# Kernel optimization log

Hardware: AMD Instinct MI355X
Metric: run time of the kernel (lower is better)

## Reference

```python
import jax, jax.numpy as jnp
import numpy as np

IMG_B, IMG_H, IMG_W, IMG_C = 16, 512, 1024, 3

def _base_grid(B, H, W):
    # replicates the module's custom normalization: arange/dim * 2 - 1
    base_x = (jnp.arange(W, dtype=jnp.float32) / W) * 2.0 - 1.0   # [W]
    base_y = (jnp.arange(H, dtype=jnp.float32) / H) * 2.0 - 1.0   # [H]
    base = jnp.stack([jnp.broadcast_to(base_x[None, :], (H, W)),
                      jnp.broadcast_to(base_y[:, None], (H, W))], axis=-1)  # [H,W,2]
    return jnp.broadcast_to(base[None], (B, H, W, 2))

def _grid_sample_bilinear_zeros(im, grid):
    # im: [B,C,H,W], grid: [B,Ho,Wo,2] in [-1,1], align_corners=False, zeros padding
    B, C, H, W = im.shape
    gx, gy = grid[..., 0], grid[..., 1]
    ix = ((gx + 1.0) * W - 1.0) * 0.5
    iy = ((gy + 1.0) * H - 1.0) * 0.5
    x0 = jnp.floor(ix); y0 = jnp.floor(iy)
    wx1 = ix - x0; wx0 = 1.0 - wx1
    wy1 = iy - y0; wy0 = 1.0 - wy1
    x0i = x0.astype(jnp.int32); y0i = y0.astype(jnp.int32)
    b_idx = jnp.arange(B, dtype=jnp.int32)[:, None, None]

    def corner(xi, yi, w):
        valid = (xi >= 0) & (xi < W) & (yi >= 0) & (yi < H)
        xc = jnp.clip(xi, 0, W - 1); yc = jnp.clip(yi, 0, H - 1)
        # advanced indexing -> [B,Ho,Wo,C]
        v = im[b_idx, :, yc, xc]
        return v * (w * valid.astype(im.dtype))[..., None]

    out = (corner(x0i,     y0i,     wx0 * wy0) +
           corner(x0i + 1, y0i,     wx1 * wy0) +
           corner(x0i,     y0i + 1, wx0 * wy1) +
           corner(x0i + 1, y0i + 1, wx1 * wy1))           # [B,Ho,Wo,C]
    return jnp.transpose(out, (0, 3, 1, 2))                # [B,C,Ho,Wo]

def setup_inputs() -> dict:
    key = jax.random.key(0)
    k1, k2, k3 = jax.random.split(key, 3)
    pred_flow = jax.random.normal(k1, (IMG_B, IMG_H, IMG_W, 2), dtype=jnp.float32) * 8.0
    im1_origin = jax.random.uniform(k2, (IMG_B, IMG_C, IMG_H, IMG_W), dtype=jnp.float32)
    im2_origin = jax.random.uniform(k3, (IMG_B, IMG_C, IMG_H, IMG_W), dtype=jnp.float32)
    return {"pred_flow": pred_flow, "im1_origin": im1_origin, "im2_origin": im2_origin}

def reference(pred_flow, im1_origin, im2_origin):
    B, H, W, _ = pred_flow.shape
    scale = jnp.array([W, H], dtype=pred_flow.dtype)
    grid = pred_flow / scale + _base_grid(B, H, W)
    im1_warp = _grid_sample_bilinear_zeros(im1_origin, grid)
    loss = jnp.sum(jnp.abs(im2_origin - im1_warp)) / (W * H)
    return loss
```

## Files before the change

kernel.cpp:

```cpp
#include <hip/hip_runtime.h>
#include <hip/hip_fp16.h>

namespace {

constexpr int B = 16, C = 3, H = 512, W = 1024;
constexpr int HW = H * W;
constexpr int SLABW = 256, SLABH = 64;
constexpr int XH  = 16;
constexpr int SWD = SLABW + 2 * XH;
constexpr int PAIRS = SWD / 2;
constexpr int PADP = 147;
constexpr int RING = 32;
constexpr int RA = 11;
constexpr int RB = 16;
constexpr int RPS = 4;
constexpr int BLOCK = 1024;
constexpr int TX = W / SLABW;
constexpr int TY = H / SLABH;
constexpr int GRID = B * TX * TY;
constexpr int PF_ROWS = RA + RB + 1;
constexpr int STG_P = C * RPS * PAIRS;
constexpr int CHS = RING * PADP;

constexpr float INV_W = 1.0f / 1024.0f;
constexpr float INV_H = 1.0f / 512.0f;

__device__ __forceinline__ float2 ld2g(const float* p) {
    struct __attribute__((packed, aligned(4))) F2 { float a, b; };
    const F2 v = *reinterpret_cast<const F2*>(p);
    return make_float2(v.a, v.b);
}

__device__ __forceinline__ uint32_t packh2(float a, float b) {
    return (uint32_t)__half_as_ushort(__float2half_rn(a))
         | ((uint32_t)__half_as_ushort(__float2half_rn(b)) << 16);
}
__device__ __forceinline__ float2 unpackh2(uint32_t u) {
    const __half2 h = __builtin_bit_cast(__half2, u);
    return make_float2(__low2float(h), __high2float(h));
}
__device__ __forceinline__ uint32_t alignsel(uint32_t hi, uint32_t lo, int sh) {
    return (uint32_t)(((((uint64_t)hi) << 32) | (uint64_t)lo) >> sh);
}

__global__ __launch_bounds__(BLOCK, 8) void flow_loss_partial(
    const float* __restrict__ flow,
    const float* __restrict__ im1,
    const float* __restrict__ im2,
    float* __restrict__ partials)
{
    __shared__ uint32_t sm32[C * CHS];
    __shared__ float red[BLOCK / 64];

    const int tid = threadIdx.x;
    const int bid = blockIdx.x;
    const int b   = bid >> 5;
    const int tt  = bid & 31;
    const int tyi = tt >> 2;
    const int txi = tt & 3;
    const int xbase  = txi * SLABW;
    const int yStart = tyi * SLABH;
    const int xb0    = xbase - XH;

    const float* __restrict__ im1b = im1 + b * C * HW;
    const float* __restrict__ im2b = im2 + b * C * HW;
    const float* __restrict__ flb  = flow + 2 * (b * HW);

    for (int e = tid; e < PF_ROWS * C * PAIRS; e += BLOCK) {
        const int q  = e % PAIRS;
        const int rc = e / PAIRS;
        const int c  = rc / PF_ROWS;
        const int ri = rc - c * PF_ROWS;
        const int row = yStart - RA + ri;
        if (row >= 0) {
            const int g0 = min(max(xb0 + 2 * q, 0), W - 1);
            const int g1 = min(max(xb0 + 2 * q + 1, 0), W - 1);
            const float a = im1b[c * HW + row * W + g0];
            const float d = im1b[c * HW + row * W + g1];
            sm32[c * CHS + (row & (RING - 1)) * PADP + q] = packh2(a, d);
        }
    }

    int  stSr[2], stG0[2], stG1[2], stL[2];
    const bool stOK1 = (tid < STG_P - BLOCK);
#pragma unroll
    for (int k = 0; k < 2; ++k) {
        const int e  = (k == 0) ? tid : (stOK1 ? BLOCK + tid : 0);
        const int q  = e % PAIRS;
        const int rc = e / PAIRS;
        const int c  = rc >> 2;
        stSr[k] = rc & 3;
        const int g0 = min(max(xb0 + 2 * q, 0), W - 1);
        const int g1 = min(max(xb0 + 2 * q + 1, 0), W - 1);
        stG0[k] = c * HW + g0;
        stG1[k] = c * HW + g1;
        stL[k]  = c * CHS + q;
    }

    auto issue = [&](int r0, int (&sIdx)[2], uint32_t (&sVal)[2]) {
#pragma unroll
        for (int k = 0; k < 2; ++k) {
            const int srow = r0 + stSr[k];
            int idx = -1; uint32_t v = 0;
            const bool act = (k == 0 || stOK1) & (srow < H);
            if (act) {
                const float a = im1b[stG0[k] + (srow << 10)];
                const float d = im1b[stG1[k] + (srow << 10)];
                v   = packh2(a, d);
                idx = stL[k] + (srow & (RING - 1)) * PADP;
            }
            sIdx[k] = idx; sVal[k] = v;
        }
    };

    int sIA[2]; uint32_t sVA[2];
    issue(yStart + RB + 1, sIA, sVA);

    const int colp = tid & (SLABW - 1);
    const int prow = tid >> 8;
    const int x = xbase + colp;
    const float base_x = (float)x * (2.0f * INV_W) - 1.0f;

    __syncthreads();

    float acc = 0.0f;

#pragma unroll 1
    for (int ys = yStart; ys < yStart + SLABH; ys += RPS) {
        int sIB[2]; uint32_t sVB[2];
        issue(ys + RB + 1 + RPS, sIB, sVB);

        const int y = ys + prow;
        const int zoff = y * W + x;
        const float2 f = *reinterpret_cast<const float2*>(flb + 2 * zoff);

        const float base_y = (float)y * (2.0f * INV_H) - 1.0f;
        const float gx = __builtin_fmaf(f.x, INV_W, base_x);
        const float gy = __builtin_fmaf(f.y, INV_H, base_y);
        const float ixf = __builtin_fmaf(gx + 1.0f, 512.0f, -0.5f);
        const float iyf = __builtin_fmaf(gy + 1.0f, 256.0f, -0.5f);

        const float x0f = floorf(ixf), y0f = floorf(iyf);
        const float wx1 = ixf - x0f, wx0 = 1.0f - wx1;
        const float wy1 = iyf - y0f, wy0 = 1.0f - wy1;
        const int x0 = (int)x0f, y0 = (int)y0f;
        const int y1 = y0 + 1;
        const bool vx0 = (x0 >= 0) & (x0 < W);
        const bool vx1 = (x0 >= -1) & (x0 < W - 1);
        const bool vy0 = (y0 >= 0) & (y0 < H);
        const bool vy1 = (y1 >= 0) & (y1 < H);
        const bool s0 = (x0 >= W - 1), s1 = (x0 >= 0);

        const float px0 = wx0 * (float)vx0;
        const float px1 = wx1 * (float)vx1;
        const float u0 = (s0 ? 0.0f : px0) + (s1 ? 0.0f : px1);
        const float u1 = (s0 ? px0 : 0.0f) + (s1 ? px1 : 0.0f);
        const float mT = wy0 * (float)vy0;
        const float mB = wy1 * (float)vy1;
        const float aT0 = mT * u0, aT1 = mT * u1;
        const float aB0 = mB * u0, aB1 = mB * u1;

        const int xL  = min(max(x0, 0), W - 2);
        const int y0c = min(max(y0, 0), H - 1);
        const int y1c = min(max(y1, 0), H - 1);

        const int jj = xL - xbase + XH;
        const bool inR = (y0c >= ys - RA) & (y1c <= ys + RB) &
                         ((unsigned)jj <= (unsigned)(SWD - 2));

        const float z0 = im2b[zoff];
        const float z1 = im2b[HW + zoff];
        const float z2 = im2b[2 * HW + zoff];

        float wp0, wp1, wp2;
        if (inR) {
            const int q  = jj >> 1;
            const int sh = (jj & 1) << 4;
            const int aT = (y0c & (RING - 1)) * PADP + q;
            const int aB = (y1c & (RING - 1)) * PADP + q;
            const uint32_t dT0a = sm32[aT],           dT0b = sm32[aT + 1];
            const uint32_t dB0a = sm32[aB],           dB0b = sm32[aB + 1];
            const uint32_t dT1a = sm32[aT + CHS],     dT1b = sm32[aT + CHS + 1];
            const uint32_t dB1a = sm32[aB + CHS],     dB1b = sm32[aB + CHS + 1];
            const uint32_t dT2a = sm32[aT + 2 * CHS], dT2b = sm32[aT + 2 * CHS + 1];
            const uint32_t dB2a = sm32[aB + 2 * CHS], dB2b = sm32[aB + 2 * CHS + 1];
            const float2 t0 = unpackh2(alignsel(dT0b, dT0a, sh));
            const float2 b0 = unpackh2(alignsel(dB0b, dB0a, sh));
            const float2 t1 = unpackh2(alignsel(dT1b, dT1a, sh));
            const float2 b1 = unpackh2(alignsel(dB1b, dB1a, sh));
            const float2 t2 = unpackh2(alignsel(dT2b, dT2a, sh));
            const float2 b2 = unpackh2(alignsel(dB2b, dB2a, sh));
            wp0 = ((aT0 * t0.x + aT1 * t0.y) + aB0 * b0.x) + aB1 * b0.y;
            wp1 = ((aT0 * t1.x + aT1 * t1.y) + aB0 * b1.x) + aB1 * b1.y;
            wp2 = ((aT0 * t2.x + aT1 * t2.y) + aB0 * b2.x) + aB1 * b2.y;
        } else {
            const int oT = y0c * W + xL, oB = y1c * W + xL;
            const float2 ta = ld2g(im1b + oT),            ba = ld2g(im1b + oB);
            const float2 tb = ld2g(im1b + HW + oT),       bb = ld2g(im1b + HW + oB);
            const float2 tc = ld2g(im1b + 2 * HW + oT),   bc = ld2g(im1b + 2 * HW + oB);
            wp0 = ((aT0 * ta.x + aT1 * ta.y) + aB0 * ba.x) + aB1 * ba.y;
            wp1 = ((aT0 * tb.x + aT1 * tb.y) + aB0 * bb.x) + aB1 * bb.y;
            wp2 = ((aT0 * tc.x + aT1 * tc.y) + aB0 * bc.x) + aB1 * bc.y;
        }
        acc += fabsf(z0 - wp0) + fabsf(z1 - wp1) + fabsf(z2 - wp2);

#pragma unroll
        for (int k = 0; k < 2; ++k)
            if (sIA[k] >= 0) sm32[sIA[k]] = sVA[k];
        __syncthreads();

#pragma unroll
        for (int k = 0; k < 2; ++k) { sIA[k] = sIB[k]; sVA[k] = sVB[k]; }
    }

#pragma unroll
    for (int o = 32; o > 0; o >>= 1)
        acc += __shfl_down(acc, o, 64);
    const int lane = tid & 63;
    const int wid  = tid >> 6;
    if (lane == 0) red[wid] = acc;
    __syncthreads();
    if (tid == 0) {
        float s = 0.0f;
#pragma unroll
        for (int wv = 0; wv < BLOCK / 64; ++wv) s += red[wv];
        partials[bid] = s;
    }
}

__global__ __launch_bounds__(256) void flow_loss_reduce(
    const float* __restrict__ partials, float* __restrict__ out)
{
    __shared__ double lds[256];
    double acc = 0.0;
    for (int i = threadIdx.x; i < GRID; i += 256) acc += (double)partials[i];
    lds[threadIdx.x] = acc;
    __syncthreads();
    for (int o = 128; o > 0; o >>= 1) {
        if (threadIdx.x < o) lds[threadIdx.x] += lds[threadIdx.x + o];
        __syncthreads();
    }
    if (threadIdx.x == 0) out[0] = (float)(lds[0] / (double)(W * H));
}

}

extern "C" void kernel_launch(void* const* d_in, const int* in_sizes, int n_in,
                              void* d_out, int out_size, void* d_ws, size_t ws_size,
                              hipStream_t stream) {
    const float* flow = (const float*)d_in[0];
    const float* im1  = (const float*)d_in[1];
    const float* im2  = (const float*)d_in[2];
    float* out = (float*)d_out;
    float* partials = (float*)d_ws;

    flow_loss_partial<<<GRID, BLOCK, 0, stream>>>(flow, im1, im2, partials);
    flow_loss_reduce<<<1, 256, 0, stream>>>(partials, out);
}
```

Before: 58.80 us.

## Interleave channels in LDS ring buffer for 128-bit loads and stores

Moves the shared-memory ring from three separate per-channel planes to an interleaved layout: each column pair holds all three channels' packed half2 values in one 16-byte slot. The bilinear gather now does four 128-bit LDS reads instead of twelve 32-bit reads, and staging and prefetch write one uint4 per pair while fetching all channels per thread. Padding the 4th word raises LDS footprint by a third and may change bank-conflict behaviour and occupancy.

```diff
diff --git a/kernel.cpp b/kernel.cpp
--- a/kernel.cpp
+++ b/kernel.cpp
@@ -9,7 +9,8 @@
 constexpr int XH  = 16;
 constexpr int SWD = SLABW + 2 * XH;
 constexpr int PAIRS = SWD / 2;
-constexpr int PADP = 147;
+constexpr int QSTR  = 4;
+constexpr int ROWSTR = PAIRS * QSTR + 4;
 constexpr int RING = 32;
 constexpr int RA = 11;
 constexpr int RB = 16;
@@ -19,8 +20,7 @@
 constexpr int TY = H / SLABH;
 constexpr int GRID = B * TX * TY;
 constexpr int PF_ROWS = RA + RB + 1;
-constexpr int STG_P = C * RPS * PAIRS;
-constexpr int CHS = RING * PADP;
+constexpr int STG_U = RPS * PAIRS;
 
 constexpr float INV_W = 1.0f / 1024.0f;
 constexpr float INV_H = 1.0f / 512.0f;
@@ -49,7 +49,7 @@
     const float* __restrict__ im2,
     float* __restrict__ partials)
 {
-    __shared__ uint32_t sm32[C * CHS];
+    __shared__ uint32_t sm32[RING * ROWSTR];
     __shared__ float red[BLOCK / 64];
 
     const int tid = threadIdx.x;
@@ -66,54 +66,60 @@
     const float* __restrict__ im2b = im2 + b * C * HW;
     const float* __restrict__ flb  = flow + 2 * (b * HW);
 
-    for (int e = tid; e < PF_ROWS * C * PAIRS; e += BLOCK) {
+    for (int e = tid; e < PF_ROWS * PAIRS; e += BLOCK) {
         const int q  = e % PAIRS;
-        const int rc = e / PAIRS;
-        const int c  = rc / PF_ROWS;
-        const int ri = rc - c * PF_ROWS;
+        const int ri = e / PAIRS;
         const int row = yStart - RA + ri;
         if (row >= 0) {
-            const int g0 = min(max(xb0 + 2 * q, 0), W - 1);
-            const int g1 = min(max(xb0 + 2 * q + 1, 0), W - 1);
-            const float a = im1b[c * HW + row * W + g0];
-            const float d = im1b[c * HW + row * W + g1];
-            sm32[c * CHS + (row & (RING - 1)) * PADP + q] = packh2(a, d);
+            const int p = xb0 + 2 * q;
+            const bool pi = (p >= 0) & (p <= W - 2);
+            const int col = pi ? p : min(max(p, 0), W - 1);
+            const float* base = im1b + row * W + col;
+            uint4 v;
+            if (pi) {
+                const float2 c0 = ld2g(base);
+                const float2 c1 = ld2g(base + HW);
+                const float2 c2 = ld2g(base + 2 * HW);
+                v = make_uint4(packh2(c0.x, c0.y), packh2(c1.x, c1.y), packh2(c2.x, c2.y), 0u);
+            } else {
+                const float a0 = *base, a1 = base[HW], a2 = base[2 * HW];
+                v = make_uint4(packh2(a0, a0), packh2(a1, a1), packh2(a2, a2), 0u);
+            }
+            *reinterpret_cast<uint4*>(sm32 + (row & (RING - 1)) * ROWSTR + q * QSTR) = v;
         }
     }
 
-    int  stSr[2], stG0[2], stG1[2], stL[2];
-    const bool stOK1 = (tid < STG_P - BLOCK);
-#pragma unroll
-    for (int k = 0; k < 2; ++k) {
-        const int e  = (k == 0) ? tid : (stOK1 ? BLOCK + tid : 0);
-        const int q  = e % PAIRS;
-        const int rc = e / PAIRS;
-        const int c  = rc >> 2;
-        stSr[k] = rc & 3;
-        const int g0 = min(max(xb0 + 2 * q, 0), W - 1);
-        const int g1 = min(max(xb0 + 2 * q + 1, 0), W - 1);
-        stG0[k] = c * HW + g0;
-        stG1[k] = c * HW + g1;
-        stL[k]  = c * CHS + q;
-    }
-
-    auto issue = [&](int r0, int (&sIdx)[2], uint32_t (&sVal)[2]) {
-#pragma unroll
-        for (int k = 0; k < 2; ++k) {
-            const int srow = r0 + stSr[k];
-            int idx = -1; uint32_t v = 0;
-            const bool act = (k == 0 || stOK1) & (srow < H);
-            if (act) {
-                const float a = im1b[stG0[k] + (srow << 10)];
-                const float d = im1b[stG1[k] + (srow << 10)];
-                v   = packh2(a, d);
-                idx = stL[k] + (srow & (RING - 1)) * PADP;
+    const bool stAct = (tid < STG_U);
+    const int  qS  = stAct ? (tid % PAIRS) : 0;
+    const int  srS = stAct ? (tid / PAIRS) : 0;
+    const int  pS  = xb0 + 2 * qS;
+    const bool stPI = (pS >= 0) & (pS <= W - 2);
+    const int  stCol = stPI ? pS : min(max(pS, 0), W - 1);
+    const int  stLq  = qS * QSTR;
+
+    auto issue = [&](int r0, int& sIdx, uint32_t (&sVal)[3]) {
+        sIdx = -1;
+        const int srow = r0 + srS;
+        if (stAct & (srow < H)) {
+            const float* base = im1b + srow * W + stCol;
+            if (stPI) {
+                const float2 c0 = ld2g(base);
+                const float2 c1 = ld2g(base + HW);
+                const float2 c2 = ld2g(base + 2 * HW);
+                sVal[0] = packh2(c0.x, c0.y);
+                sVal[1] = packh2(c1.x, c1.y);
+                sVal[2] = packh2(c2.x, c2.y);
+            } else {
+                const float a0 = *base, a1 = base[HW], a2 = base[2 * HW];
+                sVal[0] = packh2(a0, a0);
+                sVal[1] = packh2(a1, a1);
+                sVal[2] = packh2(a2, a2);
             }
-            sIdx[k] = idx; sVal[k] = v;
+            sIdx = (srow & (RING - 1)) * ROWSTR + stLq;
         }
     };
 
-    int sIA[2]; uint32_t sVA[2];
+    int sIA; uint32_t sVA[3];
     issue(yStart + RB + 1, sIA, sVA);
 
     const int colp = tid & (SLABW - 1);
@@ -127,7 +133,7 @@
 
 #pragma unroll 1
     for (int ys = yStart; ys < yStart + SLABH; ys += RPS) {
-        int sIB[2]; uint32_t sVB[2];
+        int sIB; uint32_t sVB[3];
         issue(ys + RB + 1 + RPS, sIB, sVB);
 
         const int y = ys + prow;
@@ -176,20 +182,18 @@
         if (inR) {
             const int q  = jj >> 1;
             const int sh = (jj & 1) << 4;
-            const int aT = (y0c & (RING - 1)) * PADP + q;
-            const int aB = (y1c & (RING - 1)) * PADP + q;
-            const uint32_t dT0a = sm32[aT],           dT0b = sm32[aT + 1];
-            const uint32_t dB0a = sm32[aB],           dB0b = sm32[aB + 1];
-            const uint32_t dT1a = sm32[aT + CHS],     dT1b = sm32[aT + CHS + 1];
-            const uint32_t dB1a = sm32[aB + CHS],     dB1b = sm32[aB + CHS + 1];
-            const uint32_t dT2a = sm32[aT + 2 * CHS], dT2b = sm32[aT + 2 * CHS + 1];
-            const uint32_t dB2a = sm32[aB + 2 * CHS], dB2b = sm32[aB + 2 * CHS + 1];
-            const float2 t0 = unpackh2(alignsel(dT0b, dT0a, sh));
-            const float2 b0 = unpackh2(alignsel(dB0b, dB0a, sh));
-            const float2 t1 = unpackh2(alignsel(dT1b, dT1a, sh));
-            const float2 b1 = unpackh2(alignsel(dB1b, dB1a, sh));
-            const float2 t2 = unpackh2(alignsel(dT2b, dT2a, sh));
-            const float2 b2 = unpackh2(alignsel(dB2b, dB2a, sh));
+            const int aT = (y0c & (RING - 1)) * ROWSTR + (q << 2);
+            const int aB = (y1c & (RING - 1)) * ROWSTR + (q << 2);
+            const uint4 Tq  = *reinterpret_cast<const uint4*>(sm32 + aT);
+            const uint4 Tq1 = *reinterpret_cast<const uint4*>(sm32 + aT + QSTR);
+            const uint4 Bq  = *reinterpret_cast<const uint4*>(sm32 + aB);
+            const uint4 Bq1 = *reinterpret_cast<const uint4*>(sm32 + aB + QSTR);
+            const float2 t0 = unpackh2(alignsel(Tq1.x, Tq.x, sh));
+            const float2 b0 = unpackh2(alignsel(Bq1.x, Bq.x, sh));
+            const float2 t1 = unpackh2(alignsel(Tq1.y, Tq.y, sh));
+            const float2 b1 = unpackh2(alignsel(Bq1.y, Bq.y, sh));
+            const float2 t2 = unpackh2(alignsel(Tq1.z, Tq.z, sh));
+            const float2 b2 = unpackh2(alignsel(Bq1.z, Bq.z, sh));
             wp0 = ((aT0 * t0.x + aT1 * t0.y) + aB0 * b0.x) + aB1 * b0.y;
             wp1 = ((aT0 * t1.x + aT1 * t1.y) + aB0 * b1.x) + aB1 * b1.y;
             wp2 = ((aT0 * t2.x + aT1 * t2.y) + aB0 * b2.x) + aB1 * b2.y;
@@ -204,13 +208,11 @@
         }
         acc += fabsf(z0 - wp0) + fabsf(z1 - wp1) + fabsf(z2 - wp2);
 
-#pragma unroll
-        for (int k = 0; k < 2; ++k)
-            if (sIA[k] >= 0) sm32[sIA[k]] = sVA[k];
+        if (sIA >= 0)
+            *reinterpret_cast<uint4*>(sm32 + sIA) = make_uint4(sVA[0], sVA[1], sVA[2], 0u);
         __syncthreads();
 
-#pragma unroll
-        for (int k = 0; k < 2; ++k) { sIA[k] = sIB[k]; sVA[k] = sVB[k]; }
+        sIA = sIB; sVA[0] = sVB[0]; sVA[1] = sVB[1]; sVA[2] = sVB[2];
     }
 
 #pragma unroll
```

New measurement: 60.50 us. 2.9% more time.
